# Kernel optimization log

Hardware: AMD Instinct MI355X
Metric: run time of the kernel (lower is better)

Reference implementation:

```python
import jax, jax.numpy as jnp
import numpy as np

LABEL_SMOOTHING = 0.1


def setup_inputs() -> dict:
    key = jax.random.key(0)
    k1, k2, k3 = jax.random.split(key, 3)
    B, N, D = 16384, 1000, 1000  # code structurally requires D == n_classes == N
    inputs = jax.random.uniform(k1, (B, D), dtype=jnp.float32)
    labels = jax.random.randint(k2, (B,), 0, N, dtype=jnp.int64)
    code_book = jax.random.uniform(k3, (N, D), dtype=jnp.float32)
    return {"inputs": inputs, "labels": labels, "code_book": code_book}


def reference(inputs, labels, code_book):
    # inputs: [B, D], code_book: [N, D], D == N (n_classes)
    n_classes = inputs.shape[1]
    # soft targets with label smoothing (same as scatter_ + smoothing)
    soft_target = jax.nn.one_hot(labels, n_classes, dtype=inputs.dtype)
    soft_target = soft_target * (1.0 - LABEL_SMOOTHING) + LABEL_SMOOTHING / n_classes
    # Hamming similarity: sum_d [o*c + (1-o)*(1-c)]  ==  o@c.T + (1-o)@(1-c).T
    # (algebraic rewrite of the [B, N, D] broadcast in the original; same math)
    similarity = (jnp.einsum("bd,nd->bn", inputs, code_book)
                  + jnp.einsum("bd,nd->bn", 1.0 - inputs, 1.0 - code_book))
    logp = jax.nn.log_softmax(similarity, axis=1)
    return jnp.mean(jnp.sum(-soft_target * logp, axis=1))
```

## Files before the change

### kernel.cpp

```cpp
#include <hip/hip_runtime.h>

typedef __attribute__((ext_vector_type(8))) short bf16x8;
typedef __attribute__((ext_vector_type(4))) float f32x4;

#define AS1 __attribute__((address_space(1)))
#define AS3 __attribute__((address_space(3)))

__device__ static inline void gl2lds16(const void* g, void* l) {
  __builtin_amdgcn_global_load_lds((const AS1 unsigned int*)g, (AS3 unsigned int*)l, 16, 0, 0);
}

__device__ static inline unsigned short f2bf(float x) {
  unsigned int u = __float_as_uint(x);
  unsigned int r = u + 0x7FFFu + ((u >> 16) & 1u);
  return (unsigned short)(r >> 16);
}

__global__ __launch_bounds__(256) void prep_inputs_k(const float* __restrict__ in,
                                                     unsigned short* __restrict__ a) {
  int idx = blockIdx.x * 256 + threadIdx.x;
  int row = idx >> 7;
  int g   = idx & 127;
  union { unsigned short u[8]; uint4 v; } pk;
  if (g < 125) {
    const float4* p = (const float4*)(in + (size_t)row * 1000 + g * 8);
    float4 v0 = p[0], v1 = p[1];
    pk.u[0] = f2bf(2.f * v0.x); pk.u[1] = f2bf(2.f * v0.y);
    pk.u[2] = f2bf(2.f * v0.z); pk.u[3] = f2bf(2.f * v0.w);
    pk.u[4] = f2bf(2.f * v1.x); pk.u[5] = f2bf(2.f * v1.y);
    pk.u[6] = f2bf(2.f * v1.z); pk.u[7] = f2bf(2.f * v1.w);
  } else {
    pk.v = make_uint4(0, 0, 0, 0);
  }
  *(uint4*)(a + ((size_t)row << 10) + (g << 3)) = pk.v;
}

__global__ __launch_bounds__(256) void prep_code_k(const float* __restrict__ cb,
                                                   unsigned short* __restrict__ b,
                                                   float* __restrict__ rowsum) {
  int n = blockIdx.x;
  int t = threadIdx.x;
  float s = 0.f;
#pragma unroll
  for (int j = 0; j < 4; ++j) {
    int c = t + j * 256;
    float v = 0.f;
    if (n < 1000 && c < 1000) v = cb[(size_t)n * 1000 + c];
    s += v;
    b[((size_t)n << 10) + c] = f2bf(v);
  }
  __shared__ float red[256];
  red[t] = s;
  __syncthreads();
  for (int o = 128; o > 0; o >>= 1) {
    if (t < o) red[t] += red[t + o];
    __syncthreads();
  }
  if (t == 0) rowsum[n] = (n < 1000) ? red[0] : 0.f;
}

__global__ __launch_bounds__(256, 2) void coding_loss_k(
    const unsigned short* __restrict__ A,
    const unsigned short* __restrict__ B,
    const float* __restrict__ rowsum,
    const int* __restrict__ labels,
    float* __restrict__ Z,
    float* __restrict__ lin) {
  __shared__ __align__(16) unsigned char lds[16384 + 8192 + 1024 + 16];
  unsigned short* Bt = (unsigned short*)lds;
  unsigned short* At = (unsigned short*)(lds + 16384);
  float* zbuf = (float*)(lds + 24576);
  float* lbuf = zbuf + 256;

  const int t    = threadIdx.x;
  const int lane = t & 63;
  const int w    = t >> 6;
  const int wr   = w >> 1;
  const int wc   = w & 1;
  const int g16  = lane >> 4;
  const int c16  = lane & 15;
  const int ct   = blockIdx.x & 3;
  const int rt   = blockIdx.x >> 2;
  const int r0   = rt << 7;
  const int c0   = ct << 8;

  size_t a_src[2]; int a_dst[2];
#pragma unroll
  for (int i = 0; i < 2; ++i) {
    int ch = i * 256 + t, row = ch >> 2;
    int sg = (ch & 3) ^ ((row >> 1) & 3);
    a_src[i] = (size_t)(r0 + row) * 1024 + sg * 8;
    a_dst[i] = ch * 8;
  }
  size_t b_src[4]; int b_dst[4];
#pragma unroll
  for (int i = 0; i < 4; ++i) {
    int ch = i * 256 + t, row = ch >> 2;
    int sg = (ch & 3) ^ ((row >> 1) & 3);
    b_src[i] = (size_t)(c0 + row) * 1024 + sg * 8;
    b_dst[i] = ch * 8;
  }

  int a_eoff[4], b_eoff[8];
#pragma unroll
  for (int mi = 0; mi < 4; ++mi) {
    int row = wr * 64 + mi * 16 + c16;
    a_eoff[mi] = row * 32 + ((g16 ^ ((row >> 1) & 3)) << 3);
  }
#pragma unroll
  for (int ni = 0; ni < 8; ++ni) {
    int row = wc * 128 + ni * 16 + c16;
    b_eoff[ni] = row * 32 + ((g16 ^ ((row >> 1) & 3)) << 3);
  }

  f32x4 acc[4][8];
#pragma unroll
  for (int mi = 0; mi < 4; ++mi)
#pragma unroll
    for (int ni = 0; ni < 8; ++ni) acc[mi][ni] = (f32x4)(0.f);

  for (int k0 = 0; k0 < 1024; k0 += 32) {
    __syncthreads();
    gl2lds16(A + a_src[0] + k0, At + a_dst[0]);
    gl2lds16(A + a_src[1] + k0, At + a_dst[1]);
#pragma unroll
    for (int i = 0; i < 4; ++i) gl2lds16(B + b_src[i] + k0, Bt + b_dst[i]);
    __syncthreads();

    bf16x8 af[4], bf[8];
#pragma unroll
    for (int mi = 0; mi < 4; ++mi) af[mi] = *(const bf16x8*)(At + a_eoff[mi]);
#pragma unroll
    for (int ni = 0; ni < 8; ++ni) bf[ni] = *(const bf16x8*)(Bt + b_eoff[ni]);
#pragma unroll
    for (int mi = 0; mi < 4; ++mi)
#pragma unroll
      for (int ni = 0; ni < 8; ++ni)
        acc[mi][ni] = __builtin_amdgcn_mfma_f32_16x16x32_bf16(af[mi], bf[ni], acc[mi][ni], 0, 0, 0);
  }

  float rs[8]; int colg[8];
#pragma unroll
  for (int ni = 0; ni < 8; ++ni) {
    colg[ni] = c0 + wc * 128 + ni * 16 + c16;
    rs[ni]   = rowsum[colg[ni]];
  }
  float lacc = 0.f;
  float ez[4][4];
#pragma unroll
  for (int mi = 0; mi < 4; ++mi)
#pragma unroll
    for (int r = 0; r < 4; ++r) {
      int labv = labels[r0 + wr * 64 + mi * 16 + g16 * 4 + r];
      float e = 0.f;
#pragma unroll
      for (int ni = 0; ni < 8; ++ni) {
        float S = acc[mi][ni][r] - rs[ni];
        e += __expf(S - 40.f);
        lacc += 1e-4f * S;
        if (colg[ni] == labv) lacc += 0.9f * S;
      }
      ez[mi][r] = e;
    }
#pragma unroll
  for (int d = 1; d < 16; d <<= 1)
#pragma unroll
    for (int mi = 0; mi < 4; ++mi)
#pragma unroll
      for (int r = 0; r < 4; ++r) ez[mi][r] += __shfl_xor(ez[mi][r], d, 64);
  if (c16 == 0) {
#pragma unroll
    for (int mi = 0; mi < 4; ++mi)
#pragma unroll
      for (int r = 0; r < 4; ++r) zbuf[w * 64 + mi * 16 + g16 * 4 + r] = ez[mi][r];
  }
#pragma unroll
  for (int d = 1; d < 64; d <<= 1) lacc += __shfl_xor(lacc, d, 64);
  if (lane == 0) lbuf[w] = lacc;
  __syncthreads();
  if (t < 128) {
    int wrl = t >> 6, rl = t & 63;
    float v = zbuf[(wrl * 2) * 64 + rl] + zbuf[(wrl * 2 + 1) * 64 + rl];
    atomicAdd(Z + r0 + wrl * 64 + rl, v);
  }
  if (t == 0) atomicAdd(lin, lbuf[0] + lbuf[1] + lbuf[2] + lbuf[3]);
}

__global__ __launch_bounds__(256) void finalize_k(const float* __restrict__ Z,
                                                  const float* __restrict__ lin,
                                                  float* __restrict__ out) {
  int t = threadIdx.x;
  int row = blockIdx.x * 256 + t;
  float v = 40.f + logf(Z[row]);
#pragma unroll
  for (int d = 1; d < 64; d <<= 1) v += __shfl_xor(v, d, 64);
  __shared__ float s[4];
  if ((t & 63) == 0) s[t >> 6] = v;
  __syncthreads();
  if (t == 0) {
    float tot = s[0] + s[1] + s[2] + s[3];
    if (blockIdx.x == 0) tot -= lin[0];
    atomicAdd(out, tot * (1.f / 16384.f));
  }
}

extern "C" void kernel_launch(void* const* d_in, const int* in_sizes, int n_in,
                              void* d_out, int out_size, void* d_ws, size_t ws_size,
                              hipStream_t stream) {
  const float* inputs = (const float*)d_in[0];
  const int* labels   = (const int*)d_in[1];
  const float* code   = (const float*)d_in[2];

  unsigned short* a_bf = (unsigned short*)d_ws;
  unsigned short* b_bf = a_bf + (size_t)16384 * 1024;
  float* rowsum        = (float*)(b_bf + (size_t)1024 * 1024);
  float* Z             = rowsum + 1024;
  float* lin           = Z + 16384;

  hipMemsetAsync(Z, 0, (16384 + 1) * sizeof(float), stream);
  hipMemsetAsync(d_out, 0, sizeof(float), stream);
  prep_inputs_k<<<8192, 256, 0, stream>>>(inputs, a_bf);
  prep_code_k<<<1024, 256, 0, stream>>>(code, b_bf, rowsum);
  coding_loss_k<<<512, 256, 0, stream>>>(a_bf, b_bf, rowsum, labels, Z, lin);
  finalize_k<<<64, 256, 0, stream>>>(Z, lin, (float*)d_out);
}
```

Before: 153.3 us.

## Use 1024-thread blocks with double-buffered LDS and per-half partial Z stores

The GEMM kernel now uses 1024-thread blocks covering 128x512 output tiles across 16 waves, so each A tile is loaded once per 512 columns instead of once per 256. The K loop double-buffers the LDS tiles, issuing loads for the next slice before the MFMAs on the current one and keeping one barrier per iteration instead of two. The per-row atomics into Z are replaced by plain stores into two per-column-half arrays, which finalize sums, and the large Z memset is dropped. The launch_bounds(1024,4) request and the roughly 84KB of LDS per block are unlikely to fit together, so only one block can run per CU. The grid also shrinks to 256 blocks, so occupancy and CU coverage may suffer.

```diff
diff --git a/kernel.cpp b/kernel.cpp
--- a/kernel.cpp
+++ b/kernel.cpp
@@ -59,53 +59,51 @@
   if (t == 0) rowsum[n] = (n < 1000) ? red[0] : 0.f;
 }
 
-__global__ __launch_bounds__(256, 2) void coding_loss_k(
+__global__ __launch_bounds__(1024, 4) void coding_loss_k(
     const unsigned short* __restrict__ A,
     const unsigned short* __restrict__ B,
     const float* __restrict__ rowsum,
     const int* __restrict__ labels,
     float* __restrict__ Z,
     float* __restrict__ lin) {
-  __shared__ __align__(16) unsigned char lds[16384 + 8192 + 1024 + 16];
-  unsigned short* Bt = (unsigned short*)lds;
-  unsigned short* At = (unsigned short*)(lds + 16384);
-  float* zbuf = (float*)(lds + 24576);
-  float* lbuf = zbuf + 256;
+  __shared__ __align__(16) unsigned char lds[84032];
+  unsigned short* buf = (unsigned short*)lds;
+  float* zbuf = (float*)(lds + 81920);
+  float* lbuf = zbuf + 512;
 
   const int t    = threadIdx.x;
   const int lane = t & 63;
   const int w    = t >> 6;
-  const int wr   = w >> 1;
-  const int wc   = w & 1;
+  const int wr   = w >> 2;
+  const int wc   = w & 3;
   const int g16  = lane >> 4;
   const int c16  = lane & 15;
-  const int ct   = blockIdx.x & 3;
-  const int rt   = blockIdx.x >> 2;
+  const int ct   = blockIdx.x & 1;
+  const int rt   = blockIdx.x >> 1;
   const int r0   = rt << 7;
-  const int c0   = ct << 8;
-
-  size_t a_src[2]; int a_dst[2];
+  const int c0   = ct << 9;
+
+  size_t a_src; int a_dst;
+  {
+    int ch = t, row = ch >> 2;
+    int sg = (ch & 3) ^ ((row >> 1) & 3);
+    a_src = (size_t)(r0 + row) * 1024 + sg * 8;
+    a_dst = 16384 + ch * 8;
+  }
+  size_t b_src[2]; int b_dst[2];
 #pragma unroll
   for (int i = 0; i < 2; ++i) {
-    int ch = i * 256 + t, row = ch >> 2;
-    int sg = (ch & 3) ^ ((row >> 1) & 3);
-    a_src[i] = (size_t)(r0 + row) * 1024 + sg * 8;
-    a_dst[i] = ch * 8;
-  }
-  size_t b_src[4]; int b_dst[4];
-#pragma unroll
-  for (int i = 0; i < 4; ++i) {
-    int ch = i * 256 + t, row = ch >> 2;
+    int ch = i * 1024 + t, row = ch >> 2;
     int sg = (ch & 3) ^ ((row >> 1) & 3);
     b_src[i] = (size_t)(c0 + row) * 1024 + sg * 8;
     b_dst[i] = ch * 8;
   }
 
-  int a_eoff[4], b_eoff[8];
-#pragma unroll
-  for (int mi = 0; mi < 4; ++mi) {
-    int row = wr * 64 + mi * 16 + c16;
-    a_eoff[mi] = row * 32 + ((g16 ^ ((row >> 1) & 3)) << 3);
+  int a_eoff[2], b_eoff[8];
+#pragma unroll
+  for (int mi = 0; mi < 2; ++mi) {
+    int row = wr * 32 + mi * 16 + c16;
+    a_eoff[mi] = 16384 + row * 32 + ((g16 ^ ((row >> 1) & 3)) << 3);
   }
 #pragma unroll
   for (int ni = 0; ni < 8; ++ni) {
@@ -113,30 +111,38 @@
     b_eoff[ni] = row * 32 + ((g16 ^ ((row >> 1) & 3)) << 3);
   }
 
-  f32x4 acc[4][8];
-#pragma unroll
-  for (int mi = 0; mi < 4; ++mi)
+  f32x4 acc[2][8];
+#pragma unroll
+  for (int mi = 0; mi < 2; ++mi)
 #pragma unroll
     for (int ni = 0; ni < 8; ++ni) acc[mi][ni] = (f32x4)(0.f);
 
+  if (t < 512) gl2lds16(A + a_src, buf + a_dst);
+  gl2lds16(B + b_src[0], buf + b_dst[0]);
+  gl2lds16(B + b_src[1], buf + b_dst[1]);
+  __syncthreads();
+
+  int p = 0;
   for (int k0 = 0; k0 < 1024; k0 += 32) {
-    __syncthreads();
-    gl2lds16(A + a_src[0] + k0, At + a_dst[0]);
-    gl2lds16(A + a_src[1] + k0, At + a_dst[1]);
-#pragma unroll
-    for (int i = 0; i < 4; ++i) gl2lds16(B + b_src[i] + k0, Bt + b_dst[i]);
-    __syncthreads();
-
-    bf16x8 af[4], bf[8];
-#pragma unroll
-    for (int mi = 0; mi < 4; ++mi) af[mi] = *(const bf16x8*)(At + a_eoff[mi]);
-#pragma unroll
-    for (int ni = 0; ni < 8; ++ni) bf[ni] = *(const bf16x8*)(Bt + b_eoff[ni]);
-#pragma unroll
-    for (int mi = 0; mi < 4; ++mi)
+    if (k0 + 32 < 1024) {
+      unsigned short* np = buf + (p ^ 1) * 20480;
+      if (t < 512) gl2lds16(A + a_src + k0 + 32, np + a_dst);
+      gl2lds16(B + b_src[0] + k0 + 32, np + b_dst[0]);
+      gl2lds16(B + b_src[1] + k0 + 32, np + b_dst[1]);
+    }
+    const unsigned short* bp = buf + p * 20480;
+    bf16x8 af[2], bf[8];
+#pragma unroll
+    for (int mi = 0; mi < 2; ++mi) af[mi] = *(const bf16x8*)(bp + a_eoff[mi]);
+#pragma unroll
+    for (int ni = 0; ni < 8; ++ni) bf[ni] = *(const bf16x8*)(bp + b_eoff[ni]);
+#pragma unroll
+    for (int mi = 0; mi < 2; ++mi)
 #pragma unroll
       for (int ni = 0; ni < 8; ++ni)
         acc[mi][ni] = __builtin_amdgcn_mfma_f32_16x16x32_bf16(af[mi], bf[ni], acc[mi][ni], 0, 0, 0);
+    __syncthreads();
+    p ^= 1;
   }
 
   float rs[8]; int colg[8];
@@ -146,12 +152,12 @@
     rs[ni]   = rowsum[colg[ni]];
   }
   float lacc = 0.f;
-  float ez[4][4];
-#pragma unroll
-  for (int mi = 0; mi < 4; ++mi)
+  float ez[2][4];
+#pragma unroll
+  for (int mi = 0; mi < 2; ++mi)
 #pragma unroll
     for (int r = 0; r < 4; ++r) {
-      int labv = labels[r0 + wr * 64 + mi * 16 + g16 * 4 + r];
+      int labv = labels[r0 + wr * 32 + mi * 16 + g16 * 4 + r];
       float e = 0.f;
 #pragma unroll
       for (int ni = 0; ni < 8; ++ni) {
@@ -165,25 +171,31 @@
 #pragma unroll
   for (int d = 1; d < 16; d <<= 1)
 #pragma unroll
-    for (int mi = 0; mi < 4; ++mi)
+    for (int mi = 0; mi < 2; ++mi)
 #pragma unroll
       for (int r = 0; r < 4; ++r) ez[mi][r] += __shfl_xor(ez[mi][r], d, 64);
   if (c16 == 0) {
 #pragma unroll
-    for (int mi = 0; mi < 4; ++mi)
-#pragma unroll
-      for (int r = 0; r < 4; ++r) zbuf[w * 64 + mi * 16 + g16 * 4 + r] = ez[mi][r];
+    for (int mi = 0; mi < 2; ++mi)
+#pragma unroll
+      for (int r = 0; r < 4; ++r) zbuf[w * 32 + mi * 16 + g16 * 4 + r] = ez[mi][r];
   }
 #pragma unroll
   for (int d = 1; d < 64; d <<= 1) lacc += __shfl_xor(lacc, d, 64);
   if (lane == 0) lbuf[w] = lacc;
   __syncthreads();
   if (t < 128) {
-    int wrl = t >> 6, rl = t & 63;
-    float v = zbuf[(wrl * 2) * 64 + rl] + zbuf[(wrl * 2 + 1) * 64 + rl];
-    atomicAdd(Z + r0 + wrl * 64 + rl, v);
-  }
-  if (t == 0) atomicAdd(lin, lbuf[0] + lbuf[1] + lbuf[2] + lbuf[3]);
+    int wrg = t >> 5, lr = t & 31;
+    float z = zbuf[(wrg * 4 + 0) * 32 + lr] + zbuf[(wrg * 4 + 1) * 32 + lr] +
+              zbuf[(wrg * 4 + 2) * 32 + lr] + zbuf[(wrg * 4 + 3) * 32 + lr];
+    Z[ct * 16384 + r0 + t] = z;
+  }
+  if (t == 0) {
+    float s = 0.f;
+#pragma unroll
+    for (int i = 0; i < 16; ++i) s += lbuf[i];
+    atomicAdd(lin, s);
+  }
 }
 
 __global__ __launch_bounds__(256) void finalize_k(const float* __restrict__ Z,
@@ -191,7 +203,7 @@
                                                   float* __restrict__ out) {
   int t = threadIdx.x;
   int row = blockIdx.x * 256 + t;
-  float v = 40.f + logf(Z[row]);
+  float v = 40.f + logf(Z[row] + Z[16384 + row]);
 #pragma unroll
   for (int d = 1; d < 64; d <<= 1) v += __shfl_xor(v, d, 64);
   __shared__ float s[4];
@@ -215,12 +227,12 @@
   unsigned short* b_bf = a_bf + (size_t)16384 * 1024;
   float* rowsum        = (float*)(b_bf + (size_t)1024 * 1024);
   float* Z             = rowsum + 1024;
-  float* lin           = Z + 16384;
-
-  hipMemsetAsync(Z, 0, (16384 + 1) * sizeof(float), stream);
+  float* lin           = Z + 2 * 16384;
+
+  hipMemsetAsync(lin, 0, sizeof(float), stream);
   hipMemsetAsync(d_out, 0, sizeof(float), stream);
   prep_inputs_k<<<8192, 256, 0, stream>>>(inputs, a_bf);
   prep_code_k<<<1024, 256, 0, stream>>>(code, b_bf, rowsum);
-  coding_loss_k<<<512, 256, 0, stream>>>(a_bf, b_bf, rowsum, labels, Z, lin);
+  coding_loss_k<<<256, 1024, 0, stream>>>(a_bf, b_bf, rowsum, labels, Z, lin);
   finalize_k<<<64, 256, 0, stream>>>(Z, lin, (float*)d_out);
 }
```

Measured after the change: 152.5 us. No clear change (-0.5%).

## Double-buffer LDS tiles in GEMM loop, replace Z atomics with per-tile partials

Applied to the files above, without the earlier changes.

The GEMM main loop now uses two LDS buffers and prefetches the next k-slice with global_load_lds while MFMAs run on the current one, so each iteration needs one barrier instead of two. The atomicAdd into Z is replaced by per-column-tile partial sums that finalize adds up, which removes the memset of Z. A new kernel also detects whether labels are int64 or int32 and converts them to int32. The larger LDS footprint (about 50KB per block) may limit occupancy, and the extra kernel adds launch cost.

```diff
diff --git a/kernel.cpp b/kernel.cpp
--- a/kernel.cpp
+++ b/kernel.cpp
@@ -59,6 +59,19 @@
   if (t == 0) rowsum[n] = (n < 1000) ? red[0] : 0.f;
 }
 
+__global__ __launch_bounds__(256) void fix_labels_k(const int* __restrict__ raw,
+                                                    int* __restrict__ labs) {
+  __shared__ int nz;
+  int t = threadIdx.x;
+  if (t == 0) nz = 0;
+  __syncthreads();
+  if (raw[2 * t + 1] != 0) atomicAdd(&nz, 1);
+  __syncthreads();
+  bool is64 = (nz < 32);
+  int row = blockIdx.x * 256 + t;
+  labs[row] = is64 ? raw[2 * row] : raw[row];
+}
+
 __global__ __launch_bounds__(256, 2) void coding_loss_k(
     const unsigned short* __restrict__ A,
     const unsigned short* __restrict__ B,
@@ -66,10 +79,9 @@
     const int* __restrict__ labels,
     float* __restrict__ Z,
     float* __restrict__ lin) {
-  __shared__ __align__(16) unsigned char lds[16384 + 8192 + 1024 + 16];
-  unsigned short* Bt = (unsigned short*)lds;
-  unsigned short* At = (unsigned short*)(lds + 16384);
-  float* zbuf = (float*)(lds + 24576);
+  __shared__ __align__(16) unsigned char lds[49152 + 1040];
+  unsigned short* buf = (unsigned short*)lds;
+  float* zbuf = (float*)(lds + 49152);
   float* lbuf = zbuf + 256;
 
   const int t    = threadIdx.x;
@@ -90,7 +102,7 @@
     int ch = i * 256 + t, row = ch >> 2;
     int sg = (ch & 3) ^ ((row >> 1) & 3);
     a_src[i] = (size_t)(r0 + row) * 1024 + sg * 8;
-    a_dst[i] = ch * 8;
+    a_dst[i] = 8192 + ch * 8;
   }
   size_t b_src[4]; int b_dst[4];
 #pragma unroll
@@ -104,13 +116,13 @@
   int a_eoff[4], b_eoff[8];
 #pragma unroll
   for (int mi = 0; mi < 4; ++mi) {
-    int row = wr * 64 + mi * 16 + c16;
-    a_eoff[mi] = row * 32 + ((g16 ^ ((row >> 1) & 3)) << 3);
+    int ar = wr * 64 + mi * 16 + c16;
+    a_eoff[mi] = 8192 + ar * 32 + ((g16 ^ ((ar >> 1) & 3)) << 3);
   }
 #pragma unroll
   for (int ni = 0; ni < 8; ++ni) {
-    int row = wc * 128 + ni * 16 + c16;
-    b_eoff[ni] = row * 32 + ((g16 ^ ((row >> 1) & 3)) << 3);
+    int br = wc * 128 + ni * 16 + c16;
+    b_eoff[ni] = br * 32 + ((g16 ^ ((br >> 1) & 3)) << 3);
   }
 
   f32x4 acc[4][8];
@@ -119,24 +131,34 @@
 #pragma unroll
     for (int ni = 0; ni < 8; ++ni) acc[mi][ni] = (f32x4)(0.f);
 
+#pragma unroll
+  for (int i = 0; i < 2; ++i) gl2lds16(A + a_src[i], buf + a_dst[i]);
+#pragma unroll
+  for (int i = 0; i < 4; ++i) gl2lds16(B + b_src[i], buf + b_dst[i]);
+  __syncthreads();
+
+  int p = 0;
   for (int k0 = 0; k0 < 1024; k0 += 32) {
-    __syncthreads();
-    gl2lds16(A + a_src[0] + k0, At + a_dst[0]);
-    gl2lds16(A + a_src[1] + k0, At + a_dst[1]);
-#pragma unroll
-    for (int i = 0; i < 4; ++i) gl2lds16(B + b_src[i] + k0, Bt + b_dst[i]);
-    __syncthreads();
-
+    if (k0 + 32 < 1024) {
+      unsigned short* np = buf + (p ^ 1) * 12288;
+#pragma unroll
+      for (int i = 0; i < 2; ++i) gl2lds16(A + a_src[i] + k0 + 32, np + a_dst[i]);
+#pragma unroll
+      for (int i = 0; i < 4; ++i) gl2lds16(B + b_src[i] + k0 + 32, np + b_dst[i]);
+    }
+    const unsigned short* bp = buf + p * 12288;
     bf16x8 af[4], bf[8];
 #pragma unroll
-    for (int mi = 0; mi < 4; ++mi) af[mi] = *(const bf16x8*)(At + a_eoff[mi]);
-#pragma unroll
-    for (int ni = 0; ni < 8; ++ni) bf[ni] = *(const bf16x8*)(Bt + b_eoff[ni]);
+    for (int mi = 0; mi < 4; ++mi) af[mi] = *(const bf16x8*)(bp + a_eoff[mi]);
+#pragma unroll
+    for (int ni = 0; ni < 8; ++ni) bf[ni] = *(const bf16x8*)(bp + b_eoff[ni]);
 #pragma unroll
     for (int mi = 0; mi < 4; ++mi)
 #pragma unroll
       for (int ni = 0; ni < 8; ++ni)
         acc[mi][ni] = __builtin_amdgcn_mfma_f32_16x16x32_bf16(af[mi], bf[ni], acc[mi][ni], 0, 0, 0);
+    __syncthreads();
+    p ^= 1;
   }
 
   float rs[8]; int colg[8];
@@ -179,9 +201,9 @@
   if (lane == 0) lbuf[w] = lacc;
   __syncthreads();
   if (t < 128) {
-    int wrl = t >> 6, rl = t & 63;
-    float v = zbuf[(wrl * 2) * 64 + rl] + zbuf[(wrl * 2 + 1) * 64 + rl];
-    atomicAdd(Z + r0 + wrl * 64 + rl, v);
+    int wrg = t >> 6, lr = t & 63;
+    float z = zbuf[(wrg * 2 + 0) * 64 + lr] + zbuf[(wrg * 2 + 1) * 64 + lr];
+    Z[ct * 16384 + r0 + t] = z;
   }
   if (t == 0) atomicAdd(lin, lbuf[0] + lbuf[1] + lbuf[2] + lbuf[3]);
 }
@@ -191,7 +213,7 @@
                                                   float* __restrict__ out) {
   int t = threadIdx.x;
   int row = blockIdx.x * 256 + t;
-  float v = 40.f + logf(Z[row]);
+  float v = 40.f + logf(Z[row] + Z[16384 + row] + Z[2 * 16384 + row] + Z[3 * 16384 + row]);
 #pragma unroll
   for (int d = 1; d < 64; d <<= 1) v += __shfl_xor(v, d, 64);
   __shared__ float s[4];
@@ -208,19 +230,21 @@
                               void* d_out, int out_size, void* d_ws, size_t ws_size,
                               hipStream_t stream) {
   const float* inputs = (const float*)d_in[0];
-  const int* labels   = (const int*)d_in[1];
+  const int* labraw   = (const int*)d_in[1];
   const float* code   = (const float*)d_in[2];
 
   unsigned short* a_bf = (unsigned short*)d_ws;
   unsigned short* b_bf = a_bf + (size_t)16384 * 1024;
   float* rowsum        = (float*)(b_bf + (size_t)1024 * 1024);
   float* Z             = rowsum + 1024;
-  float* lin           = Z + 16384;
-
-  hipMemsetAsync(Z, 0, (16384 + 1) * sizeof(float), stream);
+  float* lin           = Z + 4 * 16384;
+  int* labs            = (int*)(lin + 1);
+
+  hipMemsetAsync(lin, 0, sizeof(float), stream);
   hipMemsetAsync(d_out, 0, sizeof(float), stream);
+  fix_labels_k<<<64, 256, 0, stream>>>(labraw, labs);
   prep_inputs_k<<<8192, 256, 0, stream>>>(inputs, a_bf);
   prep_code_k<<<1024, 256, 0, stream>>>(code, b_bf, rowsum);
-  coding_loss_k<<<512, 256, 0, stream>>>(a_bf, b_bf, rowsum, labels, Z, lin);
+  coding_loss_k<<<512, 256, 0, stream>>>(a_bf, b_bf, rowsum, labs, Z, lin);
   finalize_k<<<64, 256, 0, stream>>>(Z, lin, (float*)d_out);
 }
```

Result: faster. 149.8 us (-2.3%).
